# Kernel tuning notes

Hardware: AMD Instinct MI355X
Metric: run time of the kernel (lower is better)

## Reference

```python
import jax, jax.numpy as jnp
import numpy as np

HIDDEN = 512
HEADS = 8
HEAD_DIM = HIDDEN // HEADS
BATCH = 4096
SEQ = 16


def setup_inputs() -> dict:
    key = jax.random.key(0)
    k1, k2, k3 = jax.random.split(key, 3)
    scale = 1.0 / np.sqrt(HIDDEN)
    return {
        "hidden_states": jax.random.normal(k1, (BATCH, SEQ, HIDDEN), dtype=jnp.float32),
        # torch Linear(hidden, 3*hidden, bias=False): weight shape [3*hidden, hidden]
        "w_qkv": jax.random.uniform(k2, (3 * HIDDEN, HIDDEN), dtype=jnp.float32, minval=-scale, maxval=scale),
        "w_o": jax.random.uniform(k3, (HIDDEN, HIDDEN), dtype=jnp.float32, minval=-scale, maxval=scale),
    }


def reference(hidden_states, w_qkv, w_o):
    b, s, _ = hidden_states.shape
    # fused QKV projection: y = x @ W^T
    qkv = jnp.einsum("bsh,oh->bso", hidden_states, w_qkv)
    qkv = qkv.reshape(b, s, 3, HEADS, HEAD_DIM)
    qkv = jnp.transpose(qkv, (2, 0, 3, 1, 4))  # [3, b, heads, s, head_dim]
    q, k, v = qkv[0], qkv[1], qkv[2]
    # scaled dot-product attention (non-causal, dropout=0 in eval)
    scores = jnp.einsum("bhqd,bhkd->bhqk", q, k) / jnp.sqrt(jnp.float32(HEAD_DIM))
    probs = jax.nn.softmax(scores, axis=-1)
    attn = jnp.einsum("bhqk,bhkd->bhqd", probs, v)
    attn = jnp.transpose(attn, (0, 2, 1, 3)).reshape(b, s, HIDDEN)
    return jnp.einsum("bsh,oh->bso", attn, w_o)
```

## Files before the change

kernel.cpp:

```cpp
#include <hip/hip_runtime.h>


#define HID 512

typedef __attribute__((ext_vector_type(4))) float  float4v;
typedef __attribute__((ext_vector_type(8))) short  short8;
typedef __attribute__((ext_vector_type(4))) short  short4v;
typedef __attribute__((ext_vector_type(8))) __bf16 bf16x8;

static __device__ __forceinline__ short bf16rne(float f) {
    union { float f; unsigned u; } v; v.f = f;
    unsigned u = v.u + 0x7FFFu + ((v.u >> 16) & 1u);
    return (short)(u >> 16);
}

static __device__ __forceinline__ short8 pack8(float4v a, float4v b) {
    short8 o;
    o[0] = bf16rne(a[0]); o[1] = bf16rne(a[1]); o[2] = bf16rne(a[2]); o[3] = bf16rne(a[3]);
    o[4] = bf16rne(b[0]); o[5] = bf16rne(b[1]); o[6] = bf16rne(b[2]); o[7] = bf16rne(b[3]);
    return o;
}

static __device__ __forceinline__ void cvt8_store(short* dst, const float* src) {
    float4v a = *(const float4v*)src;
    float4v b = *(const float4v*)(src + 4);
    *(short8*)dst = pack8(a, b);
}

static __device__ __forceinline__ void cvt4_store(short* dst, const float* src) {
    float4v v = *(const float4v*)src;
    short4v o;
    o[0] = bf16rne(v[0]); o[1] = bf16rne(v[1]); o[2] = bf16rne(v[2]); o[3] = bf16rne(v[3]);
    *(short4v*)dst = o;
}

static __device__ __forceinline__ float4v mfma16(short8 a, short8 b, float4v c) {
    union { short8 s; bf16x8 v; } ua, ub;
    ua.s = a; ub.s = b;
    return __builtin_amdgcn_mfma_f32_16x16x32_bf16(ua.v, ub.v, c, 0, 0, 0);
}

static __device__ __forceinline__ void gld16(const short* g, short* l) {
    __builtin_amdgcn_global_load_lds(
        (const __attribute__((address_space(1))) void*)g,
        (__attribute__((address_space(3))) void*)l,
        16, 0, 0);
}

__global__ void prep_kernel(const float* __restrict__ x, short* __restrict__ xb,
                            const float* __restrict__ wqkv, short* __restrict__ wqb,
                            const float* __restrict__ wo, short* __restrict__ wob,
                            const int wo_frag, const int b_wq, const int b_wo) {
    const int blk = blockIdx.x, tid = threadIdx.x;
    if (blk < b_wq) {
        const size_t i = (size_t)blk * 256 + tid;
        cvt4_store(&xb[i * 4], &x[i * 4]);
    } else if (blk < b_wo) {
        const size_t i = (size_t)(blk - b_wq) * 256 + tid;
        cvt4_store(&wqb[i * 4], &wqkv[i * 4]);
    } else if (wo_frag) {
        const int i = (blk - b_wo) * 256 + tid;
        const int lane = i & 63; int t = i >> 6;
        const int gg = t & 7; t >>= 3;
        const int ks = t & 1; t >>= 1;
        const int kb = t & 7; const int nt = t >> 3;
        const int row = nt * 128 + gg * 16 + (lane & 15);
        const int col = kb * 64 + ks * 32 + (lane >> 4) * 8;
        cvt8_store(&wob[(size_t)i * 8], &wo[(size_t)row * HID + col]);
    } else {
        const size_t i = (size_t)(blk - b_wo) * 256 + tid;
        cvt4_store(&wob[i * 4], &wo[i * 4]);
    }
}

__global__ __launch_bounds__(512, 4)
void qkv_head_kernel(const float* __restrict__ x, const short* __restrict__ xb, const int use_xb,
                     const float* __restrict__ wqf, const short* __restrict__ wqb, const int use_wb,
                     short* __restrict__ attnb, float* __restrict__ attnf, const int use_ab) {
    __shared__ __align__(16) union {
        struct { short a[2][128 * 64]; short b[2][192 * 64]; } st;
        struct { short q[128 * 72]; short k[128 * 72]; short vt[64 * 152]; short p[8 * 16 * 40]; } at;
    } L;

    const int tid  = threadIdx.x;
    const int wave = tid >> 6;
    const int lane = tid & 63;
    const int ln   = lane & 15;
    const int q8   = (lane >> 4) * 8;
    const int qrow = (lane >> 4) * 4;
    const int wr   = wave >> 2;
    const int wc   = wave & 3;

    const int g   = blockIdx.x;
    const int xcd = g & 7;
    const int j   = g >> 3;
    const int h   = j & 7;
    const int mt  = (j >> 3) * 8 + xcd;
    const int m0  = mt * 128;

    float4v acc[4][3];
    #pragma unroll
    for (int fr = 0; fr < 4; ++fr)
        #pragma unroll
        for (int fc = 0; fc < 3; ++fc)
            acc[fr][fc] = (float4v){0.f, 0.f, 0.f, 0.f};

    auto stageA = [&](int buf, int kb) {
        if (use_xb) {
            #pragma unroll
            for (int i = 0; i < 2; ++i) {
                const int cg  = i * 512 + tid;
                const int row = cg >> 3;
                const int c8  = ((cg & 7) ^ (row & 7)) * 8;
                gld16(&xb[(size_t)(m0 + row) * HID + kb * 64 + c8],
                      &L.st.a[buf][(i * 512 + (wave << 6)) * 8]);
            }
        } else {
            #pragma unroll
            for (int i = 0; i < 2; ++i) {
                const int cg  = i * 512 + tid;
                const int row = cg >> 3;
                const int c8  = ((cg & 7) ^ (row & 7)) * 8;
                cvt8_store(&L.st.a[buf][cg * 8], &x[(size_t)(m0 + row) * HID + kb * 64 + c8]);
            }
        }
    };
    auto stageB = [&](int buf, int kb) {
        if (use_wb) {
            #pragma unroll
            for (int i = 0; i < 3; ++i) {
                const int cg   = i * 512 + tid;
                const int n    = cg >> 3;
                const int c8   = ((cg & 7) ^ (n & 7)) * 8;
                const int grow = (n >> 6) * HID + h * 64 + (n & 63);
                gld16(&wqb[(size_t)grow * HID + kb * 64 + c8],
                      &L.st.b[buf][(i * 512 + (wave << 6)) * 8]);
            }
        } else {
            #pragma unroll
            for (int i = 0; i < 3; ++i) {
                const int cg   = i * 512 + tid;
                const int n    = cg >> 3;
                const int c8   = ((cg & 7) ^ (n & 7)) * 8;
                const int grow = (n >> 6) * HID + h * 64 + (n & 63);
                cvt8_store(&L.st.b[buf][cg * 8], &wqf[(size_t)grow * HID + kb * 64 + c8]);
            }
        }
    };

    stageA(0, 0);
    stageB(0, 0);
    __syncthreads();

    int cur = 0;
    for (int kb = 0; kb < 8; ++kb) {
        if (kb < 7) {
            stageA(cur ^ 1, kb + 1);
            stageB(cur ^ 1, kb + 1);
        }
        #pragma unroll
        for (int ks = 0; ks < 2; ++ks) {
            const int cslot = ks * 4 + (lane >> 4);
            short8 a[4], b[3];
            #pragma unroll
            for (int fr = 0; fr < 4; ++fr) {
                const int row = wr * 64 + fr * 16 + ln;
                a[fr] = *(const short8*)&L.st.a[cur][row * 64 + ((cslot ^ (row & 7)) << 3)];
            }
            #pragma unroll
            for (int fc = 0; fc < 3; ++fc) {
                const int row = wc * 48 + fc * 16 + ln;
                b[fc] = *(const short8*)&L.st.b[cur][row * 64 + ((cslot ^ (row & 7)) << 3)];
            }
            #pragma unroll
            for (int fr = 0; fr < 4; ++fr)
                #pragma unroll
                for (int fc = 0; fc < 3; ++fc)
                    acc[fr][fc] = mfma16(a[fr], b[fc], acc[fr][fc]);
        }
        __syncthreads();
        cur ^= 1;
    }

    #pragma unroll
    for (int fr = 0; fr < 4; ++fr) {
        #pragma unroll
        for (int fc = 0; fc < 3; ++fc) {
            const int nb = wc * 48 + fc * 16;
            const int n  = nb + ln;
            const int mb = wr * 64 + fr * 16 + qrow;
            const float4v v = acc[fr][fc];
            if (nb < 64) {
                #pragma unroll
                for (int r = 0; r < 4; ++r)
                    L.at.q[(mb + r) * 72 + n] = bf16rne(v[r] * 0.125f);
            } else if (nb < 128) {
                #pragma unroll
                for (int r = 0; r < 4; ++r)
                    L.at.k[(mb + r) * 72 + (n - 64)] = bf16rne(v[r]);
            } else {
                #pragma unroll
                for (int r = 0; r < 4; ++r)
                    L.at.vt[(n - 128) * 152 + mb + r] = bf16rne(v[r]);
            }
        }
    }
    for (int i = tid; i < 64 * 24; i += 512)
        L.at.vt[(i / 24) * 152 + 128 + (i % 24)] = 0;
    for (int i = tid; i < 8 * 16 * 16; i += 512)
        L.at.p[(i >> 8) * 640 + ((i >> 4) & 15) * 40 + 16 + (i & 15)] = 0;
    __syncthreads();

    {
        const int rb = wave * 16;
        const short* qp = &L.at.q[(rb + ln) * 72 + q8];
        const short* kp = &L.at.k[(rb + ln) * 72 + q8];
        short8 aq0 = *(const short8*)qp;
        short8 aq1 = *(const short8*)(qp + 32);
        short8 bk0 = *(const short8*)kp;
        short8 bk1 = *(const short8*)(kp + 32);
        float4v s = (float4v){0.f, 0.f, 0.f, 0.f};
        s = mfma16(aq0, bk0, s);
        s = mfma16(aq1, bk1, s);

        float4v mx = s;
        #pragma unroll
        for (int off = 1; off < 16; off <<= 1)
            #pragma unroll
            for (int r = 0; r < 4; ++r)
                mx[r] = fmaxf(mx[r], __shfl_xor(mx[r], off));
        float4v p;
        #pragma unroll
        for (int r = 0; r < 4; ++r) p[r] = __expf(s[r] - mx[r]);
        float4v sm = p;
        #pragma unroll
        for (int off = 1; off < 16; off <<= 1)
            #pragma unroll
            for (int r = 0; r < 4; ++r)
                sm[r] += __shfl_xor(sm[r], off);
        #pragma unroll
        for (int r = 0; r < 4; ++r)
            L.at.p[wave * 640 + (qrow + r) * 40 + ln] = bf16rne(p[r] * __builtin_amdgcn_rcpf(sm[r]));

        short8 ap = *(const short8*)&L.at.p[wave * 640 + ln * 40 + q8];
        #pragma unroll
        for (int dc = 0; dc < 4; ++dc) {
            short8 bv = *(const short8*)&L.at.vt[(dc * 16 + ln) * 152 + rb + q8];
            float4v o = (float4v){0.f, 0.f, 0.f, 0.f};
            o = mfma16(ap, bv, o);
            #pragma unroll
            for (int r = 0; r < 4; ++r) {
                const size_t oi = (size_t)(m0 + rb + qrow + r) * HID + h * 64 + dc * 16 + ln;
                if (use_ab) attnb[oi] = bf16rne(o[r]);
                else        attnf[oi] = o[r];
            }
        }
    }
}

__global__ __launch_bounds__(256, 3)
void oproj_kernel(const short* __restrict__ attnb, const short* __restrict__ wob,
                  float* __restrict__ out) {
    __shared__ __align__(16) short A[2][128 * 64];

    const int tid  = threadIdx.x;
    const int wave = tid >> 6;
    const int lane = tid & 63;
    const int ln   = lane & 15;
    const int qrow = (lane >> 4) * 4;
    const int wr   = wave >> 1;
    const int wc   = wave & 1;

    const int g   = blockIdx.x;
    const int xcd = g & 7;
    const int j   = g >> 3;
    const int nt  = j & 3;
    const int mt  = (j >> 2) * 8 + xcd;
    const int m0  = mt * 128;
    const int n0  = nt * 128;

    float4v acc[4][4];
    #pragma unroll
    for (int fr = 0; fr < 4; ++fr)
        #pragma unroll
        for (int fc = 0; fc < 4; ++fc)
            acc[fr][fc] = (float4v){0.f, 0.f, 0.f, 0.f};

    auto stageA = [&](int buf, int kb) {
        #pragma unroll
        for (int i = 0; i < 4; ++i) {
            const int cg  = i * 256 + tid;
            const int row = cg >> 3;
            const int c8  = ((cg & 7) ^ (row & 7)) * 8;
            gld16(&attnb[(size_t)(m0 + row) * HID + kb * 64 + c8],
                  &A[buf][(i * 256 + (wave << 6)) * 8]);
        }
    };
    auto loadKs = [&](short8* d, int kb, int ks) {
        #pragma unroll
        for (int fc = 0; fc < 4; ++fc) {
            const int chunk = ((nt * 8 + kb) * 2 + ks) * 8 + wc * 4 + fc;
            d[fc] = *(const short8*)&wob[(size_t)chunk * 512 + lane * 8];
        }
    };

    short8 bf[4][4];
    loadKs(bf[0], 0, 0);
    loadKs(bf[1], 0, 1);
    stageA(0, 0);
    __syncthreads();

    #pragma unroll
    for (int kb = 0; kb < 8; ++kb) {
        const int cur = kb & 1;
        const int s0 = (2 * kb) & 3, s1 = (2 * kb + 1) & 3;
        const int t0 = (2 * kb + 2) & 3, t1 = (2 * kb + 3) & 3;
        if (kb < 7) {
            stageA(cur ^ 1, kb + 1);
            loadKs(bf[t0], kb + 1, 0);
            loadKs(bf[t1], kb + 1, 1);
        }
        {
            const int cslot = (lane >> 4);
            short8 a[4];
            #pragma unroll
            for (int fr = 0; fr < 4; ++fr) {
                const int row = wr * 64 + fr * 16 + ln;
                a[fr] = *(const short8*)&A[cur][row * 64 + ((cslot ^ (row & 7)) << 3)];
            }
            #pragma unroll
            for (int fr = 0; fr < 4; ++fr)
                #pragma unroll
                for (int fc = 0; fc < 4; ++fc)
                    acc[fr][fc] = mfma16(a[fr], bf[s0][fc], acc[fr][fc]);
        }
        {
            const int cslot = 4 + (lane >> 4);
            short8 a[4];
            #pragma unroll
            for (int fr = 0; fr < 4; ++fr) {
                const int row = wr * 64 + fr * 16 + ln;
                a[fr] = *(const short8*)&A[cur][row * 64 + ((cslot ^ (row & 7)) << 3)];
            }
            #pragma unroll
            for (int fr = 0; fr < 4; ++fr)
                #pragma unroll
                for (int fc = 0; fc < 4; ++fc)
                    acc[fr][fc] = mfma16(a[fr], bf[s1][fc], acc[fr][fc]);
        }
        __syncthreads();
    }

    #pragma unroll
    for (int fr = 0; fr < 4; ++fr)
        #pragma unroll
        for (int fc = 0; fc < 4; ++fc)
            #pragma unroll
            for (int r = 0; r < 4; ++r)
                out[(size_t)(m0 + wr * 64 + fr * 16 + qrow + r) * HID +
                    n0 + wc * 64 + fc * 16 + ln] = acc[fr][fc][r];
}

__global__ __launch_bounds__(512, 2)
void oproj_inplace_kernel(float* __restrict__ io, const float* __restrict__ wof,
                          const short* __restrict__ wob, const int use_wb) {
    __shared__ __align__(16) short sA[64 * 40];
    __shared__ __align__(16) short sW2[512 * 40];

    const int tid  = threadIdx.x;
    const int wave = tid >> 6;
    const int lane = tid & 63;
    const int ln   = lane & 15;
    const int q8   = (lane >> 4) * 8;
    const int qrow = (lane >> 4) * 4;
    const int m0   = blockIdx.x * 64;

    float4v acc[4][4];
    #pragma unroll
    for (int fr = 0; fr < 4; ++fr)
        #pragma unroll
        for (int fc = 0; fc < 4; ++fc)
            acc[fr][fc] = (float4v){0.f, 0.f, 0.f, 0.f};

    for (int kb = 0; kb < 16; ++kb) {
        __syncthreads();
        if (tid < 256) {
            int row = tid >> 2, c8 = (tid & 3) * 8;
            cvt8_store(&sA[row * 40 + c8], &io[(size_t)(m0 + row) * HID + kb * 32 + c8]);
        }
        #pragma unroll
        for (int it = 0; it < 4; ++it) {
            int gg = tid + it * 512;
            int n = gg >> 2, c8 = (gg & 3) * 8;
            if (use_wb)
                *(short8*)&sW2[n * 40 + c8] = *(const short8*)&wob[(size_t)n * HID + kb * 32 + c8];
            else
                cvt8_store(&sW2[n * 40 + c8], &wof[(size_t)n * HID + kb * 32 + c8]);
        }
        __syncthreads();
        short8 a[4], b[4];
        #pragma unroll
        for (int fr = 0; fr < 4; ++fr)
            a[fr] = *(const short8*)&sA[(fr * 16 + ln) * 40 + q8];
        #pragma unroll
        for (int fc = 0; fc < 4; ++fc)
            b[fc] = *(const short8*)&sW2[(wave * 64 + fc * 16 + ln) * 40 + q8];
        #pragma unroll
        for (int fr = 0; fr < 4; ++fr)
            #pragma unroll
            for (int fc = 0; fc < 4; ++fc)
                acc[fr][fc] = mfma16(a[fr], b[fc], acc[fr][fc]);
    }
    #pragma unroll
    for (int fr = 0; fr < 4; ++fr)
        #pragma unroll
        for (int fc = 0; fc < 4; ++fc)
            #pragma unroll
            for (int r = 0; r < 4; ++r)
                io[(size_t)(m0 + fr * 16 + qrow + r) * HID + wave * 64 + fc * 16 + ln] =
                    acc[fr][fc][r];
}

extern "C" void kernel_launch(void* const* d_in, const int* in_sizes, int n_in,
                              void* d_out, int out_size, void* d_ws, size_t ws_size,
                              hipStream_t stream) {
    const float* x    = (const float*)d_in[0];
    const float* wqkv = (const float*)d_in[1];
    const float* wo   = (const float*)d_in[2];
    float* out = (float*)d_out;

    const size_t n_x  = (size_t)65536 * HID;
    const size_t n_wq = (size_t)1536 * HID;
    const size_t n_wo = (size_t)HID * HID;
    const size_t szA = (n_x * 2 + n_wq + n_wo) * 2;
    const size_t szB = (n_x + n_wq + n_wo) * 2;
    const size_t szC = (n_wq + n_wo) * 2;

    short* xb = nullptr; short* attnb = nullptr; short* wqb = nullptr; short* wob = nullptr;
    int use_xb = 0, use_ab = 0, use_wb = 0;
    short* ws = (short*)d_ws;

    if (d_ws && ws_size >= szA) {
        use_xb = use_ab = use_wb = 1;
        xb = ws; attnb = xb + n_x; wqb = attnb + n_x; wob = wqb + n_wq;
    } else if (d_ws && ws_size >= szB) {
        use_ab = use_wb = 1;
        attnb = ws; wqb = attnb + n_x; wob = wqb + n_wq;
    } else if (d_ws && ws_size >= szC) {
        use_wb = 1;
        wqb = ws; wob = wqb + n_wq;
    }

    if (use_wb) {
        const int nbx = use_xb ? 32768 : 0;
        const int b_wq = nbx;
        const int b_wo = nbx + 768;
        const int wo_frag = use_ab ? 1 : 0;
        const int grid = b_wo + (wo_frag ? 128 : 256);
        prep_kernel<<<grid, 256, 0, stream>>>(x, xb, wqkv, wqb, wo, wob,
                                              wo_frag, b_wq, b_wo);
    }

    qkv_head_kernel<<<4096, 512, 0, stream>>>(x, xb, use_xb, wqkv, wqb, use_wb,
                                              attnb, out , use_ab);

    if (use_ab)
        oproj_kernel<<<2048, 256, 0, stream>>>(attnb, wob, out);
    else
        oproj_inplace_kernel<<<1024, 512, 0, stream>>>(out, wo, wob, use_wb);
}
```

Baseline: 372.8 us.

## Drop bf16 pre-conversion of activations; load fp32 into registers and convert in-loop

Removes the separate prep pass that converted the whole fp32 activation tensor to bf16 in workspace. The QKV kernel now loads fp32 activations into registers before the MFMA work for the current tile and packs and writes them to LDS afterwards, overlapping global latency with compute. This avoids writing and re-reading a 64 MB bf16 copy, but each head block (8 per row tile) now reads fp32 activations, doubling per-block A traffic and adding conversion ALU and register pressure.

```diff
diff --git a/kernel.cpp b/kernel.cpp
--- a/kernel.cpp
+++ b/kernel.cpp
@@ -47,16 +47,12 @@
         16, 0, 0);
 }
 
-__global__ void prep_kernel(const float* __restrict__ x, short* __restrict__ xb,
-                            const float* __restrict__ wqkv, short* __restrict__ wqb,
+__global__ void prep_kernel(const float* __restrict__ wqkv, short* __restrict__ wqb,
                             const float* __restrict__ wo, short* __restrict__ wob,
-                            const int wo_frag, const int b_wq, const int b_wo) {
+                            const int wo_frag, const int b_wo) {
     const int blk = blockIdx.x, tid = threadIdx.x;
-    if (blk < b_wq) {
+    if (blk < b_wo) {
         const size_t i = (size_t)blk * 256 + tid;
-        cvt4_store(&xb[i * 4], &x[i * 4]);
-    } else if (blk < b_wo) {
-        const size_t i = (size_t)(blk - b_wq) * 256 + tid;
         cvt4_store(&wqb[i * 4], &wqkv[i * 4]);
     } else if (wo_frag) {
         const int i = (blk - b_wo) * 256 + tid;
@@ -74,7 +70,7 @@
 }
 
 __global__ __launch_bounds__(512, 4)
-void qkv_head_kernel(const float* __restrict__ x, const short* __restrict__ xb, const int use_xb,
+void qkv_head_kernel(const float* __restrict__ x,
                      const float* __restrict__ wqf, const short* __restrict__ wqb, const int use_wb,
                      short* __restrict__ attnb, float* __restrict__ attnf, const int use_ab) {
     __shared__ __align__(16) union {
@@ -105,24 +101,23 @@
         for (int fc = 0; fc < 3; ++fc)
             acc[fr][fc] = (float4v){0.f, 0.f, 0.f, 0.f};
 
-    auto stageA = [&](int buf, int kb) {
-        if (use_xb) {
-            #pragma unroll
-            for (int i = 0; i < 2; ++i) {
-                const int cg  = i * 512 + tid;
-                const int row = cg >> 3;
-                const int c8  = ((cg & 7) ^ (row & 7)) * 8;
-                gld16(&xb[(size_t)(m0 + row) * HID + kb * 64 + c8],
-                      &L.st.a[buf][(i * 512 + (wave << 6)) * 8]);
-            }
-        } else {
-            #pragma unroll
-            for (int i = 0; i < 2; ++i) {
-                const int cg  = i * 512 + tid;
-                const int row = cg >> 3;
-                const int c8  = ((cg & 7) ^ (row & 7)) * 8;
-                cvt8_store(&L.st.a[buf][cg * 8], &x[(size_t)(m0 + row) * HID + kb * 64 + c8]);
-            }
+    float4v areg[2][2];
+    auto loadA = [&](int kb) {
+        #pragma unroll
+        for (int i = 0; i < 2; ++i) {
+            const int cg  = i * 512 + tid;
+            const int row = cg >> 3;
+            const int c8  = ((cg & 7) ^ (row & 7)) * 8;
+            const float* s = &x[(size_t)(m0 + row) * HID + kb * 64 + c8];
+            areg[i][0] = *(const float4v*)s;
+            areg[i][1] = *(const float4v*)(s + 4);
+        }
+    };
+    auto writeA = [&](int buf) {
+        #pragma unroll
+        for (int i = 0; i < 2; ++i) {
+            const int cg = i * 512 + tid;
+            *(short8*)&L.st.a[buf][cg * 8] = pack8(areg[i][0], areg[i][1]);
         }
     };
     auto stageB = [&](int buf, int kb) {
@@ -148,14 +143,15 @@
         }
     };
 
-    stageA(0, 0);
+    loadA(0);
+    writeA(0);
     stageB(0, 0);
     __syncthreads();
 
     int cur = 0;
     for (int kb = 0; kb < 8; ++kb) {
         if (kb < 7) {
-            stageA(cur ^ 1, kb + 1);
+            loadA(kb + 1);
             stageB(cur ^ 1, kb + 1);
         }
         #pragma unroll
@@ -178,6 +174,7 @@
                 for (int fc = 0; fc < 3; ++fc)
                     acc[fr][fc] = mfma16(a[fr], b[fc], acc[fr][fc]);
         }
+        if (kb < 7) writeA(cur ^ 1);
         __syncthreads();
         cur ^= 1;
     }
@@ -432,18 +429,14 @@
     const size_t n_x  = (size_t)65536 * HID;
     const size_t n_wq = (size_t)1536 * HID;
     const size_t n_wo = (size_t)HID * HID;
-    const size_t szA = (n_x * 2 + n_wq + n_wo) * 2;
     const size_t szB = (n_x + n_wq + n_wo) * 2;
     const size_t szC = (n_wq + n_wo) * 2;
 
-    short* xb = nullptr; short* attnb = nullptr; short* wqb = nullptr; short* wob = nullptr;
-    int use_xb = 0, use_ab = 0, use_wb = 0;
+    short* attnb = nullptr; short* wqb = nullptr; short* wob = nullptr;
+    int use_ab = 0, use_wb = 0;
     short* ws = (short*)d_ws;
 
-    if (d_ws && ws_size >= szA) {
-        use_xb = use_ab = use_wb = 1;
-        xb = ws; attnb = xb + n_x; wqb = attnb + n_x; wob = wqb + n_wq;
-    } else if (d_ws && ws_size >= szB) {
+    if (d_ws && ws_size >= szB) {
         use_ab = use_wb = 1;
         attnb = ws; wqb = attnb + n_x; wob = wqb + n_wq;
     } else if (d_ws && ws_size >= szC) {
@@ -452,16 +445,13 @@
     }
 
     if (use_wb) {
-        const int nbx = use_xb ? 32768 : 0;
-        const int b_wq = nbx;
-        const int b_wo = nbx + 768;
+        const int b_wo = 768;
         const int wo_frag = use_ab ? 1 : 0;
         const int grid = b_wo + (wo_frag ? 128 : 256);
-        prep_kernel<<<grid, 256, 0, stream>>>(x, xb, wqkv, wqb, wo, wob,
-                                              wo_frag, b_wq, b_wo);
-    }
-
-    qkv_head_kernel<<<4096, 512, 0, stream>>>(x, xb, use_xb, wqkv, wqb, use_wb,
+        prep_kernel<<<grid, 256, 0, stream>>>(wqkv, wqb, wo, wob, wo_frag, b_wo);
+    }
+
+    qkv_head_kernel<<<4096, 512, 0, stream>>>(x, wqkv, wqb, use_wb,
                                               attnb, out , use_ab);
 
     if (use_ab)
```

Result: slower. 394.2 us (+5.7%).
